# Performance work log

Hardware: AMD Instinct MI355X
Metric: run time of the kernel (lower is better)

Reference implementation:

```python
import jax, jax.numpy as jnp
import numpy as np

B, L, D_IN, D_OUT, H = 2, 2048, 1024, 1024, 16
HD = D_OUT // H


def setup_inputs() -> dict:
    key = jax.random.key(0)
    ks = jax.random.split(key, 7)
    s_in = 1.0 / np.sqrt(D_IN)
    s_out = 1.0 / np.sqrt(D_OUT)
    return {
        "x": jax.random.normal(ks[0], (B, L, D_IN), dtype=jnp.float32),
        "Wq": jax.random.uniform(ks[1], (D_OUT, D_IN), jnp.float32, -s_in, s_in),
        "Wg": jax.random.uniform(ks[2], (D_OUT, D_IN), jnp.float32, -s_in, s_in),
        "Wk": jax.random.uniform(ks[3], (D_OUT, D_IN), jnp.float32, -s_in, s_in),
        "Wv": jax.random.uniform(ks[4], (D_OUT, D_IN), jnp.float32, -s_in, s_in),
        "Wo": jax.random.uniform(ks[5], (D_OUT, D_OUT), jnp.float32, -s_out, s_out),
        "bo": jax.random.uniform(ks[6], (D_OUT,), jnp.float32, -s_out, s_out),
    }


def reference(x, Wq, Wg, Wk, Wv, Wo, bo):
    b, l, _ = x.shape
    # projections (torch Linear: x @ W^T)
    q = jnp.einsum('bld,od->blo', x, Wq).reshape(b, l, H, HD)
    g = jnp.einsum('bld,od->blo', x, Wg)
    k = jnp.einsum('bld,od->blo', x, Wk).reshape(b, l, H, HD)
    v = jnp.einsum('bld,od->blo', x, Wv).reshape(b, l, H, HD)
    # attention scores [B,H,L,L]
    scores = jnp.einsum('bqhd,bkhd->bhqk', q, k)
    causal = jnp.tril(jnp.ones((l, l), dtype=bool))
    neg = jnp.finfo(scores.dtype).min
    scores = jnp.where(causal[None, None], scores, neg)
    attn = jax.nn.softmax(scores / np.sqrt(HD), axis=-1)
    ctx = jnp.einsum('bhqk,bkhd->bqhd', attn, v).reshape(b, l, D_OUT)
    ctx = ctx * jax.nn.sigmoid(g)
    return jnp.einsum('blo,po->blp', ctx, Wo) + bo
```

## Files before the change

kernel.cpp:

```cpp
#include <hip/hip_runtime.h>
#include <hip/hip_bf16.h>


typedef __bf16 v8bf __attribute__((ext_vector_type(8)));
typedef __bf16 v4bf __attribute__((ext_vector_type(4)));
typedef float  v4f  __attribute__((ext_vector_type(4)));

using gas_void = const __attribute__((address_space(1))) void*;
using las_void = __attribute__((address_space(3))) void*;

__device__ __forceinline__ void async_ld16(const void* g, void* l) {
  __builtin_amdgcn_global_load_lds((gas_void)g, (las_void)l, 16, 0, 0);
}
__device__ __forceinline__ float fexp2(float x) { return __builtin_amdgcn_exp2f(x); }

#define QSCALE 0.18033688011112042f
#define LOG2E  1.4426950408889634f
#define FIXMAX 8.0f

__global__ void cvt_all_kernel(const float* __restrict__ x,  const float* __restrict__ Wq,
                               const float* __restrict__ Wg, const float* __restrict__ Wk,
                               const float* __restrict__ Wv, const float* __restrict__ Wo,
                               __bf16* __restrict__ xb, __bf16* __restrict__ w3,
                               __bf16* __restrict__ wvb, __bf16* __restrict__ wob) {
  const int i0 = blockIdx.x * 512 + threadIdx.x;
#pragma unroll
  for (int rep = 0; rep < 2; ++rep) {
    const int i = i0 + rep * 256;
    const float* s; v4bf* d; int j; float sc = 1.f;
    if (i < 1048576)      { s = x;  d = (v4bf*)xb;           j = i; }
    else if (i < 1310720) { s = Wq; d = (v4bf*)w3;           j = i - 1048576; sc = QSCALE; }
    else if (i < 1572864) { s = Wg; d = (v4bf*)w3 + 262144;  j = i - 1310720; }
    else if (i < 1835008) { s = Wk; d = (v4bf*)w3 + 524288;  j = i - 1572864; }
    else if (i < 2097152) { s = Wv; d = (v4bf*)wvb;          j = i - 1835008; }
    else                  { s = Wo; d = (v4bf*)wob;          j = i - 2097152; }
    float4 v = reinterpret_cast<const float4*>(s)[j];
    v4bf o;
    o[0] = (__bf16)(v.x * sc); o[1] = (__bf16)(v.y * sc);
    o[2] = (__bf16)(v.z * sc); o[3] = (__bf16)(v.w * sc);
    d[j] = o;
  }
}

template<bool OUTF32, int BN>
__device__ __forceinline__ void gemm_tile(
    const __bf16* __restrict__ A, const __bf16* __restrict__ B,
    void* __restrict__ C, const float* __restrict__ bias,
    int K, int lda, int ldb, int ldc, int m0, int n0,
    __bf16* As, __bf16* Bs) {
  constexpr int NI = BN / 32;
  const int tid  = threadIdx.x;
  const int w    = tid >> 6;
  const int lane = tid & 63;
  const int fr   = lane & 15;
  const int fq   = lane >> 4;
  const int sr   = lane >> 3;
  const int sc   = lane & 7;
  const int wr = (w >> 1) * 64, wc = (w & 1) * (BN / 2);

  v4f acc[4][NI];
#pragma unroll
  for (int i = 0; i < 4; ++i)
#pragma unroll
    for (int j = 0; j < NI; ++j)
#pragma unroll
      for (int r = 0; r < 4; ++r) acc[i][j][r] = 0.f;

  auto stage = [&](int bi, int k0) {
#pragma unroll
    for (int i = 0; i < 4; ++i) {
      const int c = w + i * 4;
      async_ld16(A + (size_t)(m0 + c * 8 + sr) * lda + k0 + ((sc ^ sr) * 8),
                 (void*)(As + bi * 8192 + c * 512));
    }
#pragma unroll
    for (int i = 0; i < BN / 32; ++i) {
      const int c = w + i * 4;
      async_ld16(B + (size_t)(n0 + c * 8 + sr) * ldb + k0 + ((sc ^ sr) * 8),
                 (void*)(Bs + bi * (BN * 64) + c * 512));
    }
  };

  const int nk = K >> 6;
  stage(0, 0);
  for (int t = 0; t < nk; ++t) {
    if (t + 1 < nk) {
      stage((t + 1) & 1, (t + 1) * 64);
      if (BN == 64) asm volatile("s_waitcnt vmcnt(6)" ::: "memory");
      else          asm volatile("s_waitcnt vmcnt(8)" ::: "memory");
    } else {
      asm volatile("s_waitcnt vmcnt(0)" ::: "memory");
    }
    __builtin_amdgcn_s_barrier();
    __builtin_amdgcn_sched_barrier(0);

    const __bf16* Ac = As + (t & 1) * 8192;
    const __bf16* Bc = Bs + (t & 1) * (BN * 64);
#pragma unroll
    for (int ks = 0; ks < 2; ++ks) {
      v8bf a[4], b[NI];
#pragma unroll
      for (int mi = 0; mi < 4; ++mi)
        a[mi] = *reinterpret_cast<const v8bf*>(
            Ac + (wr + mi * 16 + fr) * 64 + (((ks * 4 + fq) ^ (fr & 7)) * 8));
#pragma unroll
      for (int ni = 0; ni < NI; ++ni)
        b[ni] = *reinterpret_cast<const v8bf*>(
            Bc + (wc + ni * 16 + fr) * 64 + (((ks * 4 + fq) ^ (fr & 7)) * 8));
      __builtin_amdgcn_s_setprio(1);
#pragma unroll
      for (int mi = 0; mi < 4; ++mi)
#pragma unroll
        for (int ni = 0; ni < NI; ++ni)
          acc[mi][ni] = __builtin_amdgcn_mfma_f32_16x16x32_bf16(a[mi], b[ni], acc[mi][ni], 0, 0, 0);
      __builtin_amdgcn_s_setprio(0);
    }
    __builtin_amdgcn_sched_barrier(0);
    __builtin_amdgcn_s_barrier();
  }

#pragma unroll
  for (int mi = 0; mi < 4; ++mi)
#pragma unroll
    for (int ni = 0; ni < NI; ++ni)
#pragma unroll
      for (int r = 0; r < 4; ++r) {
        const int row = m0 + wr + mi * 16 + fq * 4 + r;
        const int col = n0 + wc + ni * 16 + fr;
        const float v = acc[mi][ni][r];
        if (OUTF32) {
          reinterpret_cast<float*>(C)[(size_t)row * ldc + col] = v + bias[col];
        } else {
          reinterpret_cast<__bf16*>(C)[(size_t)row * ldc + col] = (__bf16)v;
        }
      }
}

__global__ __launch_bounds__(256) void proj_kernel(
    const __bf16* __restrict__ xb, const __bf16* __restrict__ w3,
    const __bf16* __restrict__ wvb, __bf16* __restrict__ qgk, __bf16* __restrict__ vt) {
  __shared__ __bf16 As[2 * 128 * 64];
  __shared__ __bf16 Bs[2 * 64 * 64];
  const int bid = blockIdx.x;
  if (bid < 1536) {
    gemm_tile<false, 64>(xb, w3, (void*)qgk, nullptr, 1024, 1024, 1024, 3072,
                         (bid / 48) * 128, (bid % 48) * 64, As, Bs);
  } else {
    const int t = bid - 1536;
    gemm_tile<false, 64>(wvb, xb, (void*)vt, nullptr, 1024, 1024, 1024, 4096,
                         (t >> 6) * 128, (t & 63) * 64, As, Bs);
  }
}

template<bool OUTF32, int BN>
__global__ __launch_bounds__(256) void gemm_bt_kernel(
    const __bf16* __restrict__ A, const __bf16* __restrict__ B,
    void* __restrict__ C, const float* __restrict__ bias,
    int K, int lda, int ldb, int ldc) {
  __shared__ __bf16 As[2 * 128 * 64];
  __shared__ __bf16 Bs[2 * BN * 64];
  gemm_tile<OUTF32, BN>(A, B, C, bias, K, lda, ldb, ldc,
                        blockIdx.y * 128, blockIdx.x * BN, As, Bs);
}

__global__ __launch_bounds__(256, 4) void attn_kernel(
    const __bf16* __restrict__ QGK, const __bf16* __restrict__ VT,
    __bf16* __restrict__ CTX) {
  constexpr int LD = 3072, L = 2048;
  __shared__ __align__(16) char lds[37888];
  const int w = threadIdx.x >> 6, lane = threadIdx.x & 63;
  const int fr = lane & 15, fq = lane >> 4;
  const int tl = w >> 1, hf = w & 1;
  const int u = blockIdx.x >> 8, v = blockIdx.x & 255;
  const int k = v >> 5;
  const int g = (u == 0) ? k : (u == 1) ? 15 - k : (u == 2) ? 16 + k : 31 - k;
  const int bh = v & 31;
  const int b = bh >> 4, h = bh & 15, hb = h * 64;
  const int qt = 2 * g + tl, q0 = qt * 32, nkt = g + 1;
  const __bf16* base  = QGK + (size_t)b * L * LD;
  const __bf16* vbase = VT + (size_t)hb * 4096 + (size_t)b * L;
  __bf16* pw = (__bf16*)(lds + 16384 + w * 2560);

  v8bf onev;
#pragma unroll
  for (int i = 0; i < 8; ++i) onev[i] = (__bf16)1.0f;

  v8bf qf[2][2];
#pragma unroll
  for (int mi = 0; mi < 2; ++mi)
#pragma unroll
    for (int ks = 0; ks < 2; ++ks)
      qf[mi][ks] = *reinterpret_cast<const v8bf*>(
          base + (size_t)(q0 + mi * 16 + fr) * LD + hb + ks * 32 + fq * 8);

  v4f cacc[2][4], csum[2];
#pragma unroll
  for (int mi = 0; mi < 2; ++mi) {
#pragma unroll
    for (int r = 0; r < 4; ++r) csum[mi][r] = 0.f;
#pragma unroll
    for (int nf = 0; nf < 4; ++nf)
#pragma unroll
      for (int r = 0; r < 4; ++r) cacc[mi][nf][r] = 0.f;
  }

  auto stage = [&](int bi, int k0s) {
    char* bf_ = (char*)lds + bi * 8192;
#pragma unroll
    for (int i = 0; i < 2; ++i) {
      const int slot = i * 256 + w * 64 + lane;
      const int r = slot >> 3;
      const int cc = ((slot & 7) ^ (r & 7)) * 8;
      async_ld16(base + (size_t)(k0s + r) * LD + 2048 + hb + cc,
                 bf_ + (i * 256 + w * 64) * 16);
    }
  };

  stage(0, 0);
  __syncthreads();
  for (int kt = 0; kt < nkt; ++kt) {
    const int k0 = kt * 64;
    const bool last = (kt == nkt - 1);
    v8bf vf[4];
#pragma unroll
    for (int nf = 0; nf < 4; ++nf)
      vf[nf] = *reinterpret_cast<const v8bf*>(
          vbase + (size_t)(nf * 16 + fr) * 4096 + k0 + hf * 32 + fq * 8);
    if (!last) stage((kt + 1) & 1, k0 + 64);

    if (!(last && tl == 0 && hf == 1)) {
      const __bf16* Kt = (const __bf16*)(lds + (kt & 1) * 8192);
      v8bf kf[2][2];
#pragma unroll
      for (int ks = 0; ks < 2; ++ks)
#pragma unroll
        for (int nj = 0; nj < 2; ++nj)
          kf[ks][nj] = *reinterpret_cast<const v8bf*>(
              Kt + (hf * 32 + nj * 16 + fr) * 64 + (((ks * 4 + fq) ^ (fr & 7)) * 8));

      v4f s[2][2];
#pragma unroll
      for (int mi = 0; mi < 2; ++mi)
#pragma unroll
        for (int nj = 0; nj < 2; ++nj)
#pragma unroll
          for (int r = 0; r < 4; ++r) s[mi][nj][r] = 0.f;
      __builtin_amdgcn_s_setprio(1);
#pragma unroll
      for (int ks = 0; ks < 2; ++ks)
#pragma unroll
        for (int mi = 0; mi < 2; ++mi)
#pragma unroll
          for (int nj = 0; nj < 2; ++nj)
            s[mi][nj] = __builtin_amdgcn_mfma_f32_16x16x32_bf16(
                kf[ks][nj], qf[mi][ks], s[mi][nj], 0, 0, 0);
      __builtin_amdgcn_s_setprio(0);

      const bool mask = last && (hf == tl);
#pragma unroll
      for (int mi = 0; mi < 2; ++mi) {
        const int qrow = q0 + mi * 16 + fr;
#pragma unroll
        for (int nj = 0; nj < 2; ++nj) {
          const int kvb = k0 + hf * 32 + nj * 16 + fq * 4;
          v4bf pk;
#pragma unroll
          for (int r = 0; r < 4; ++r) {
            float sv = s[mi][nj][r];
            if (mask && (kvb + r > qrow)) sv = -__builtin_inff();
            pk[r] = (__bf16)fexp2(sv - FIXMAX);
          }
          *reinterpret_cast<v4bf*>(pw + (mi * 16 + fr) * 40 + nj * 16 + fq * 4) = pk;
        }
      }

      v8bf pa[2];
#pragma unroll
      for (int mi = 0; mi < 2; ++mi)
        pa[mi] = *reinterpret_cast<const v8bf*>(pw + (mi * 16 + fr) * 40 + fq * 8);
      __builtin_amdgcn_s_setprio(1);
#pragma unroll
      for (int mi = 0; mi < 2; ++mi)
        csum[mi] = __builtin_amdgcn_mfma_f32_16x16x32_bf16(pa[mi], onev, csum[mi], 0, 0, 0);
#pragma unroll
      for (int nf = 0; nf < 4; ++nf)
#pragma unroll
        for (int mi = 0; mi < 2; ++mi)
          cacc[mi][nf] = __builtin_amdgcn_mfma_f32_16x16x32_bf16(pa[mi], vf[nf], cacc[mi][nf], 0, 0, 0);
      __builtin_amdgcn_s_setprio(0);
    }
    __syncthreads();
  }

  float* comb = (float*)(lds + 16384);
  float* slot = comb + (tl * 64 + lane) * 41;
  if (hf == 1) {
#pragma unroll
    for (int mi = 0; mi < 2; ++mi) {
#pragma unroll
      for (int nf = 0; nf < 4; ++nf)
#pragma unroll
        for (int r = 0; r < 4; ++r) slot[mi * 16 + nf * 4 + r] = cacc[mi][nf][r];
#pragma unroll
      for (int r = 0; r < 4; ++r) slot[32 + mi * 4 + r] = csum[mi][r];
    }
  }
  __syncthreads();
  if (hf == 0) {
#pragma unroll
    for (int mi = 0; mi < 2; ++mi) {
#pragma unroll
      for (int nf = 0; nf < 4; ++nf)
#pragma unroll
        for (int r = 0; r < 4; ++r) cacc[mi][nf][r] += slot[mi * 16 + nf * 4 + r];
#pragma unroll
      for (int r = 0; r < 4; ++r) csum[mi][r] += slot[32 + mi * 4 + r];
    }
#pragma unroll
    for (int mi = 0; mi < 2; ++mi)
#pragma unroll
      for (int r = 0; r < 4; ++r) {
        const int grow = q0 + mi * 16 + fq * 4 + r;
        const float rl = 1.f / csum[mi][r];
#pragma unroll
        for (int nf = 0; nf < 4; ++nf) {
          const int col = hb + nf * 16 + fr;
          float vv = cacc[mi][nf][r] * rl;
          const float gt = (float)base[(size_t)grow * LD + 1024 + col];
          vv *= 1.f / (1.f + fexp2(-gt * LOG2E));
          CTX[((size_t)b * L + grow) * 1024 + col] = (__bf16)vv;
        }
      }
  }
}

extern "C" void kernel_launch(void* const* d_in, const int* in_sizes, int n_in,
                              void* d_out, int out_size, void* d_ws, size_t ws_size,
                              hipStream_t stream) {
  const float* x  = (const float*)d_in[0];
  const float* Wq = (const float*)d_in[1];
  const float* Wg = (const float*)d_in[2];
  const float* Wk = (const float*)d_in[3];
  const float* Wv = (const float*)d_in[4];
  const float* Wo = (const float*)d_in[5];
  const float* bo = (const float*)d_in[6];

  char* ws = (char*)d_ws;
  __bf16* xb  = (__bf16*)(ws);
  __bf16* w3  = (__bf16*)(ws + (8u  << 20));
  __bf16* wvb = (__bf16*)(ws + (14u << 20));
  __bf16* wob = (__bf16*)(ws + (16u << 20));
  __bf16* qgk = (__bf16*)(ws + (18u << 20));
  __bf16* vt  = (__bf16*)(ws + (42u << 20));
  __bf16* ctx = (__bf16*)(ws + (50u << 20));

  cvt_all_kernel<<<dim3(4608), dim3(256), 0, stream>>>(x, Wq, Wg, Wk, Wv, Wo,
                                                       xb, w3, wvb, wob);

  proj_kernel<<<dim3(2048), dim3(256), 0, stream>>>(xb, w3, wvb, qgk, vt);

  attn_kernel<<<dim3(1024), dim3(256), 0, stream>>>(qgk, vt, ctx);

  gemm_bt_kernel<true, 64><<<dim3(16, 32), dim3(256), 0, stream>>>(
      ctx, wob, d_out, bo, 1024, 1024, 1024, 1024);
}
```

Before: 119.9 us.

## Halve attention query tile and add a small-tile output GEMM

Each attention block now handles 32 query rows with 16 per wave pair instead of 64. The grid doubles to 2048 blocks, ordered so the longest causal tiles start first, and LDS shrinks so six blocks fit per CU. The output projection becomes a dedicated 64x64-tile kernel with 1024 blocks, single-buffered, replacing the 128x64 double-buffered template GEMM. Both changes aim at better load balance and CU occupancy, at the cost of fewer MFMAs per K/V load, more redundant K/V staging, and no load/compute overlap in the output GEMM.

```diff
diff --git a/kernel.cpp b/kernel.cpp
--- a/kernel.cpp
+++ b/kernel.cpp
@@ -152,57 +152,109 @@
   }
 }
 
-template<bool OUTF32, int BN>
-__global__ __launch_bounds__(256) void gemm_bt_kernel(
+__global__ __launch_bounds__(256) void gemm_out_kernel(
     const __bf16* __restrict__ A, const __bf16* __restrict__ B,
-    void* __restrict__ C, const float* __restrict__ bias,
-    int K, int lda, int ldb, int ldc) {
-  __shared__ __bf16 As[2 * 128 * 64];
-  __shared__ __bf16 Bs[2 * BN * 64];
-  gemm_tile<OUTF32, BN>(A, B, C, bias, K, lda, ldb, ldc,
-                        blockIdx.y * 128, blockIdx.x * BN, As, Bs);
-}
-
-__global__ __launch_bounds__(256, 4) void attn_kernel(
+    float* __restrict__ C, const float* __restrict__ bias) {
+  __shared__ __bf16 As[64 * 64];
+  __shared__ __bf16 Bs[64 * 64];
+  const int tid  = threadIdx.x;
+  const int w    = tid >> 6;
+  const int lane = tid & 63;
+  const int fr   = lane & 15;
+  const int fq   = lane >> 4;
+  const int sr   = lane >> 3;
+  const int sc   = lane & 7;
+  const int m0 = blockIdx.y * 64, n0 = blockIdx.x * 64;
+  const int wr = (w >> 1) * 32, wc = (w & 1) * 32;
+
+  v4f acc[2][2];
+#pragma unroll
+  for (int i = 0; i < 2; ++i)
+#pragma unroll
+    for (int j = 0; j < 2; ++j)
+#pragma unroll
+      for (int r = 0; r < 4; ++r) acc[i][j][r] = 0.f;
+
+  for (int k0 = 0; k0 < 1024; k0 += 64) {
+#pragma unroll
+    for (int i = 0; i < 2; ++i) {
+      const int c = w + i * 4;
+      async_ld16(A + (size_t)(m0 + c * 8 + sr) * 1024 + k0 + ((sc ^ sr) * 8),
+                 (void*)(As + c * 512));
+      async_ld16(B + (size_t)(n0 + c * 8 + sr) * 1024 + k0 + ((sc ^ sr) * 8),
+                 (void*)(Bs + c * 512));
+    }
+    __syncthreads();
+
+#pragma unroll
+    for (int ks = 0; ks < 2; ++ks) {
+      v8bf a[2], b[2];
+#pragma unroll
+      for (int mi = 0; mi < 2; ++mi)
+        a[mi] = *reinterpret_cast<const v8bf*>(
+            As + (wr + mi * 16 + fr) * 64 + (((ks * 4 + fq) ^ (fr & 7)) * 8));
+#pragma unroll
+      for (int ni = 0; ni < 2; ++ni)
+        b[ni] = *reinterpret_cast<const v8bf*>(
+            Bs + (wc + ni * 16 + fr) * 64 + (((ks * 4 + fq) ^ (fr & 7)) * 8));
+      __builtin_amdgcn_s_setprio(1);
+#pragma unroll
+      for (int mi = 0; mi < 2; ++mi)
+#pragma unroll
+        for (int ni = 0; ni < 2; ++ni)
+          acc[mi][ni] = __builtin_amdgcn_mfma_f32_16x16x32_bf16(a[mi], b[ni], acc[mi][ni], 0, 0, 0);
+      __builtin_amdgcn_s_setprio(0);
+    }
+    __syncthreads();
+  }
+
+#pragma unroll
+  for (int mi = 0; mi < 2; ++mi)
+#pragma unroll
+    for (int ni = 0; ni < 2; ++ni)
+#pragma unroll
+      for (int r = 0; r < 4; ++r) {
+        const int row = m0 + wr + mi * 16 + fq * 4 + r;
+        const int col = n0 + wc + ni * 16 + fr;
+        C[(size_t)row * 1024 + col] = acc[mi][ni][r] + bias[col];
+      }
+}
+
+__global__ __launch_bounds__(256, 6) void attn_kernel(
     const __bf16* __restrict__ QGK, const __bf16* __restrict__ VT,
     __bf16* __restrict__ CTX) {
   constexpr int LD = 3072, L = 2048;
-  __shared__ __align__(16) char lds[37888];
+  __shared__ __align__(16) char lds[21504];
   const int w = threadIdx.x >> 6, lane = threadIdx.x & 63;
   const int fr = lane & 15, fq = lane >> 4;
-  const int tl = w >> 1, hf = w & 1;
-  const int u = blockIdx.x >> 8, v = blockIdx.x & 255;
-  const int k = v >> 5;
-  const int g = (u == 0) ? k : (u == 1) ? 15 - k : (u == 2) ? 16 + k : 31 - k;
-  const int bh = v & 31;
+  const int mh = w >> 1, hf = w & 1;
+  const int bid = blockIdx.x;
+  const int qt = 63 - (bid >> 5);
+  const int bh = bid & 31;
   const int b = bh >> 4, h = bh & 15, hb = h * 64;
-  const int qt = 2 * g + tl, q0 = qt * 32, nkt = g + 1;
+  const int q0 = qt * 32;
+  const int nkt = (qt >> 1) + 1;
   const __bf16* base  = QGK + (size_t)b * L * LD;
   const __bf16* vbase = VT + (size_t)hb * 4096 + (size_t)b * L;
-  __bf16* pw = (__bf16*)(lds + 16384 + w * 2560);
+  __bf16* pw = (__bf16*)(lds + 16384 + w * 1280);
 
   v8bf onev;
 #pragma unroll
   for (int i = 0; i < 8; ++i) onev[i] = (__bf16)1.0f;
 
-  v8bf qf[2][2];
-#pragma unroll
-  for (int mi = 0; mi < 2; ++mi)
-#pragma unroll
-    for (int ks = 0; ks < 2; ++ks)
-      qf[mi][ks] = *reinterpret_cast<const v8bf*>(
-          base + (size_t)(q0 + mi * 16 + fr) * LD + hb + ks * 32 + fq * 8);
-
-  v4f cacc[2][4], csum[2];
-#pragma unroll
-  for (int mi = 0; mi < 2; ++mi) {
-#pragma unroll
-    for (int r = 0; r < 4; ++r) csum[mi][r] = 0.f;
-#pragma unroll
-    for (int nf = 0; nf < 4; ++nf)
-#pragma unroll
-      for (int r = 0; r < 4; ++r) cacc[mi][nf][r] = 0.f;
-  }
+  v8bf qf[2];
+#pragma unroll
+  for (int ks = 0; ks < 2; ++ks)
+    qf[ks] = *reinterpret_cast<const v8bf*>(
+        base + (size_t)(q0 + mh * 16 + fr) * LD + hb + ks * 32 + fq * 8);
+
+  v4f cacc[4], csum;
+#pragma unroll
+  for (int r = 0; r < 4; ++r) csum[r] = 0.f;
+#pragma unroll
+  for (int nf = 0; nf < 4; ++nf)
+#pragma unroll
+    for (int r = 0; r < 4; ++r) cacc[nf][r] = 0.f;
 
   auto stage = [&](int bi, int k0s) {
     char* bf_ = (char*)lds + bi * 8192;
@@ -228,7 +280,7 @@
           vbase + (size_t)(nf * 16 + fr) * 4096 + k0 + hf * 32 + fq * 8);
     if (!last) stage((kt + 1) & 1, k0 + 64);
 
-    if (!(last && tl == 0 && hf == 1)) {
+    if (!(last && !(qt & 1) && hf == 1)) {
       const __bf16* Kt = (const __bf16*)(lds + (kt & 1) * 8192);
       v8bf kf[2][2];
 #pragma unroll
@@ -238,99 +290,76 @@
           kf[ks][nj] = *reinterpret_cast<const v8bf*>(
               Kt + (hf * 32 + nj * 16 + fr) * 64 + (((ks * 4 + fq) ^ (fr & 7)) * 8));
 
-      v4f s[2][2];
-#pragma unroll
-      for (int mi = 0; mi < 2; ++mi)
+      v4f s[2];
+#pragma unroll
+      for (int nj = 0; nj < 2; ++nj)
+#pragma unroll
+        for (int r = 0; r < 4; ++r) s[nj][r] = 0.f;
+      __builtin_amdgcn_s_setprio(1);
+#pragma unroll
+      for (int ks = 0; ks < 2; ++ks)
 #pragma unroll
         for (int nj = 0; nj < 2; ++nj)
-#pragma unroll
-          for (int r = 0; r < 4; ++r) s[mi][nj][r] = 0.f;
+          s[nj] = __builtin_amdgcn_mfma_f32_16x16x32_bf16(kf[ks][nj], qf[ks], s[nj], 0, 0, 0);
+      __builtin_amdgcn_s_setprio(0);
+
+      const bool mask = last && (hf == (qt & 1));
+      const int qrow = q0 + mh * 16 + fr;
+#pragma unroll
+      for (int nj = 0; nj < 2; ++nj) {
+        const int kvb = k0 + hf * 32 + nj * 16 + fq * 4;
+        v4bf pk;
+#pragma unroll
+        for (int r = 0; r < 4; ++r) {
+          float sv = s[nj][r];
+          if (mask && (kvb + r > qrow)) sv = -__builtin_inff();
+          pk[r] = (__bf16)fexp2(sv - FIXMAX);
+        }
+        *reinterpret_cast<v4bf*>(pw + fr * 40 + nj * 16 + fq * 4) = pk;
+      }
+
+      const v8bf pa = *reinterpret_cast<const v8bf*>(pw + fr * 40 + fq * 8);
       __builtin_amdgcn_s_setprio(1);
-#pragma unroll
-      for (int ks = 0; ks < 2; ++ks)
-#pragma unroll
-        for (int mi = 0; mi < 2; ++mi)
-#pragma unroll
-          for (int nj = 0; nj < 2; ++nj)
-            s[mi][nj] = __builtin_amdgcn_mfma_f32_16x16x32_bf16(
-                kf[ks][nj], qf[mi][ks], s[mi][nj], 0, 0, 0);
+      csum = __builtin_amdgcn_mfma_f32_16x16x32_bf16(pa, onev, csum, 0, 0, 0);
+#pragma unroll
+      for (int nf = 0; nf < 4; ++nf)
+        cacc[nf] = __builtin_amdgcn_mfma_f32_16x16x32_bf16(pa, vf[nf], cacc[nf], 0, 0, 0);
       __builtin_amdgcn_s_setprio(0);
-
-      const bool mask = last && (hf == tl);
-#pragma unroll
-      for (int mi = 0; mi < 2; ++mi) {
-        const int qrow = q0 + mi * 16 + fr;
-#pragma unroll
-        for (int nj = 0; nj < 2; ++nj) {
-          const int kvb = k0 + hf * 32 + nj * 16 + fq * 4;
-          v4bf pk;
-#pragma unroll
-          for (int r = 0; r < 4; ++r) {
-            float sv = s[mi][nj][r];
-            if (mask && (kvb + r > qrow)) sv = -__builtin_inff();
-            pk[r] = (__bf16)fexp2(sv - FIXMAX);
-          }
-          *reinterpret_cast<v4bf*>(pw + (mi * 16 + fr) * 40 + nj * 16 + fq * 4) = pk;
-        }
-      }
-
-      v8bf pa[2];
-#pragma unroll
-      for (int mi = 0; mi < 2; ++mi)
-        pa[mi] = *reinterpret_cast<const v8bf*>(pw + (mi * 16 + fr) * 40 + fq * 8);
-      __builtin_amdgcn_s_setprio(1);
-#pragma unroll
-      for (int mi = 0; mi < 2; ++mi)
-        csum[mi] = __builtin_amdgcn_mfma_f32_16x16x32_bf16(pa[mi], onev, csum[mi], 0, 0, 0);
-#pragma unroll
-      for (int nf = 0; nf < 4; ++nf)
-#pragma unroll
-        for (int mi = 0; mi < 2; ++mi)
-          cacc[mi][nf] = __builtin_amdgcn_mfma_f32_16x16x32_bf16(pa[mi], vf[nf], cacc[mi][nf], 0, 0, 0);
-      __builtin_amdgcn_s_setprio(0);
     }
     __syncthreads();
   }
 
-  float* comb = (float*)(lds + 16384);
-  float* slot = comb + (tl * 64 + lane) * 41;
+  float* comb = (float*)lds;
+  float* slot = comb + (mh * 64 + lane) * 21;
   if (hf == 1) {
 #pragma unroll
-    for (int mi = 0; mi < 2; ++mi) {
-#pragma unroll
-      for (int nf = 0; nf < 4; ++nf)
-#pragma unroll
-        for (int r = 0; r < 4; ++r) slot[mi * 16 + nf * 4 + r] = cacc[mi][nf][r];
-#pragma unroll
-      for (int r = 0; r < 4; ++r) slot[32 + mi * 4 + r] = csum[mi][r];
-    }
+    for (int nf = 0; nf < 4; ++nf)
+#pragma unroll
+      for (int r = 0; r < 4; ++r) slot[nf * 4 + r] = cacc[nf][r];
+#pragma unroll
+    for (int r = 0; r < 4; ++r) slot[16 + r] = csum[r];
   }
   __syncthreads();
   if (hf == 0) {
 #pragma unroll
-    for (int mi = 0; mi < 2; ++mi) {
-#pragma unroll
-      for (int nf = 0; nf < 4; ++nf)
-#pragma unroll
-        for (int r = 0; r < 4; ++r) cacc[mi][nf][r] += slot[mi * 16 + nf * 4 + r];
-#pragma unroll
-      for (int r = 0; r < 4; ++r) csum[mi][r] += slot[32 + mi * 4 + r];
-    }
-#pragma unroll
-    for (int mi = 0; mi < 2; ++mi)
-#pragma unroll
-      for (int r = 0; r < 4; ++r) {
-        const int grow = q0 + mi * 16 + fq * 4 + r;
-        const float rl = 1.f / csum[mi][r];
-#pragma unroll
-        for (int nf = 0; nf < 4; ++nf) {
-          const int col = hb + nf * 16 + fr;
-          float vv = cacc[mi][nf][r] * rl;
-          const float gt = (float)base[(size_t)grow * LD + 1024 + col];
-          vv *= 1.f / (1.f + fexp2(-gt * LOG2E));
-          CTX[((size_t)b * L + grow) * 1024 + col] = (__bf16)vv;
-        }
+    for (int nf = 0; nf < 4; ++nf)
+#pragma unroll
+      for (int r = 0; r < 4; ++r) cacc[nf][r] += slot[nf * 4 + r];
+#pragma unroll
+    for (int r = 0; r < 4; ++r) csum[r] += slot[16 + r];
+#pragma unroll
+    for (int r = 0; r < 4; ++r) {
+      const int grow = q0 + mh * 16 + fq * 4 + r;
+      const float rl = 1.f / csum[r];
+#pragma unroll
+      for (int nf = 0; nf < 4; ++nf) {
+        const int col = hb + nf * 16 + fr;
+        float vv = cacc[nf][r] * rl;
+        const float gt = (float)base[(size_t)grow * LD + 1024 + col];
+        vv *= 1.f / (1.f + fexp2(-gt * LOG2E));
+        CTX[((size_t)b * L + grow) * 1024 + col] = (__bf16)vv;
       }
+    }
   }
 }
 
@@ -359,8 +388,7 @@
 
   proj_kernel<<<dim3(2048), dim3(256), 0, stream>>>(xb, w3, wvb, qgk, vt);
 
-  attn_kernel<<<dim3(1024), dim3(256), 0, stream>>>(qgk, vt, ctx);
-
-  gemm_bt_kernel<true, 64><<<dim3(16, 32), dim3(256), 0, stream>>>(
-      ctx, wob, d_out, bo, 1024, 1024, 1024, 1024);
-}
+  attn_kernel<<<dim3(2048), dim3(256), 0, stream>>>(qgk, vt, ctx);
+
+  gemm_out_kernel<<<dim3(16, 64), dim3(256), 0, stream>>>(ctx, wob, (float*)d_out, bo);
+}
```

Result: slower. 206.5 us (+72.2%).

## Use dedicated 64x64-tile single-buffered kernel for output projection

Applied to the files above, without the earlier changes.

Replaces the generic 128x64 double-buffered GEMM for the output projection with a specialized 64x64 tile kernel. The grid doubles to 1024 blocks, which fills the many CUs better for this 4096x1024x1024 GEMM. It also uses a smaller LDS footprint with XOR-swizzled async loads and setprio around MFMAs. The trade-off is that single buffering exposes load latency at each k-step, and smaller tiles lower operand reuse.

```diff
diff --git a/kernel.cpp b/kernel.cpp
--- a/kernel.cpp
+++ b/kernel.cpp
@@ -152,15 +152,72 @@
   }
 }
 
-template<bool OUTF32, int BN>
-__global__ __launch_bounds__(256) void gemm_bt_kernel(
+__global__ __launch_bounds__(256) void gemm_out_kernel(
     const __bf16* __restrict__ A, const __bf16* __restrict__ B,
-    void* __restrict__ C, const float* __restrict__ bias,
-    int K, int lda, int ldb, int ldc) {
-  __shared__ __bf16 As[2 * 128 * 64];
-  __shared__ __bf16 Bs[2 * BN * 64];
-  gemm_tile<OUTF32, BN>(A, B, C, bias, K, lda, ldb, ldc,
-                        blockIdx.y * 128, blockIdx.x * BN, As, Bs);
+    float* __restrict__ C, const float* __restrict__ bias) {
+  __shared__ __bf16 As[64 * 64];
+  __shared__ __bf16 Bs[64 * 64];
+  const int tid  = threadIdx.x;
+  const int w    = tid >> 6;
+  const int lane = tid & 63;
+  const int fr   = lane & 15;
+  const int fq   = lane >> 4;
+  const int sr   = lane >> 3;
+  const int sc   = lane & 7;
+  const int m0 = blockIdx.y * 64, n0 = blockIdx.x * 64;
+  const int wr = (w >> 1) * 32, wc = (w & 1) * 32;
+
+  v4f acc[2][2];
+#pragma unroll
+  for (int i = 0; i < 2; ++i)
+#pragma unroll
+    for (int j = 0; j < 2; ++j)
+#pragma unroll
+      for (int r = 0; r < 4; ++r) acc[i][j][r] = 0.f;
+
+  for (int k0 = 0; k0 < 1024; k0 += 64) {
+#pragma unroll
+    for (int i = 0; i < 2; ++i) {
+      const int c = w + i * 4;
+      async_ld16(A + (size_t)(m0 + c * 8 + sr) * 1024 + k0 + ((sc ^ sr) * 8),
+                 (void*)(As + c * 512));
+      async_ld16(B + (size_t)(n0 + c * 8 + sr) * 1024 + k0 + ((sc ^ sr) * 8),
+                 (void*)(Bs + c * 512));
+    }
+    __syncthreads();
+
+#pragma unroll
+    for (int ks = 0; ks < 2; ++ks) {
+      v8bf a[2], b[2];
+#pragma unroll
+      for (int mi = 0; mi < 2; ++mi)
+        a[mi] = *reinterpret_cast<const v8bf*>(
+            As + (wr + mi * 16 + fr) * 64 + (((ks * 4 + fq) ^ (fr & 7)) * 8));
+#pragma unroll
+      for (int ni = 0; ni < 2; ++ni)
+        b[ni] = *reinterpret_cast<const v8bf*>(
+            Bs + (wc + ni * 16 + fr) * 64 + (((ks * 4 + fq) ^ (fr & 7)) * 8));
+      __builtin_amdgcn_s_setprio(1);
+#pragma unroll
+      for (int mi = 0; mi < 2; ++mi)
+#pragma unroll
+        for (int ni = 0; ni < 2; ++ni)
+          acc[mi][ni] = __builtin_amdgcn_mfma_f32_16x16x32_bf16(a[mi], b[ni], acc[mi][ni], 0, 0, 0);
+      __builtin_amdgcn_s_setprio(0);
+    }
+    __syncthreads();
+  }
+
+#pragma unroll
+  for (int mi = 0; mi < 2; ++mi)
+#pragma unroll
+    for (int ni = 0; ni < 2; ++ni)
+#pragma unroll
+      for (int r = 0; r < 4; ++r) {
+        const int row = m0 + wr + mi * 16 + fq * 4 + r;
+        const int col = n0 + wc + ni * 16 + fr;
+        C[(size_t)row * 1024 + col] = acc[mi][ni][r] + bias[col];
+      }
 }
 
 __global__ __launch_bounds__(256, 4) void attn_kernel(
@@ -361,6 +418,5 @@
 
   attn_kernel<<<dim3(1024), dim3(256), 0, stream>>>(qgk, vt, ctx);
 
-  gemm_bt_kernel<true, 64><<<dim3(16, 32), dim3(256), 0, stream>>>(
-      ctx, wob, d_out, bo, 1024, 1024, 1024, 1024);
-}
+  gemm_out_kernel<<<dim3(16, 64), dim3(256), 0, stream>>>(ctx, wob, (float*)d_out, bo);
+}
```

Result: no change. 119.9 us (+0.0%).
